# Optimization experiments

Measured on AMD Instinct MI355X. Metric: run time of the kernel, lower is better.

The kernel has to match this reference:

```python
import jax, jax.numpy as jnp
import numpy as np

B, T, D = 2, 2048, 2048
H = 16
D_HEAD = D // H          # 128
D_SUB = D_HEAD // 2      # 64
SCALE = float(np.sqrt(D_SUB))


def setup_inputs() -> dict:
    key = jax.random.key(0)
    ks = jax.random.split(key, 6)
    s = 1.0 / np.sqrt(D)
    return {
        "x": jax.random.normal(ks[0], (B, T, D), dtype=jnp.float32),
        "W_q": jax.random.normal(ks[1], (D, D), dtype=jnp.float32) * s,
        "W_k": jax.random.normal(ks[2], (D, D), dtype=jnp.float32) * s,
        "W_v": jax.random.normal(ks[3], (D, D), dtype=jnp.float32) * s,
        "W_o": jax.random.normal(ks[4], (D, D), dtype=jnp.float32) * s,
        "lambda_param": jnp.full((H,), 0.8, dtype=jnp.float32),
    }


def reference(x, W_q, W_k, W_v, W_o, lambda_param):
    # Linear layers (torch nn.Linear: x @ W.T), reshape to heads
    Q = (x @ W_q.T).reshape(B, T, H, D_HEAD)
    K = (x @ W_k.T).reshape(B, T, H, D_HEAD)
    V = (x @ W_v.T).reshape(B, T, H, D_HEAD)
    # split each head into two sub-heads
    Q1, Q2 = Q[..., :D_SUB], Q[..., D_SUB:2 * D_SUB]
    K1, K2 = K[..., :D_SUB], K[..., D_SUB:2 * D_SUB]
    # dual attention maps: [B, H, T, T]
    attn1 = jnp.einsum('bthd,bshd->bhts', Q1, K1) / SCALE
    attn2 = jnp.einsum('bthd,bshd->bhts', Q2, K2) / SCALE
    A1 = jax.nn.softmax(attn1, axis=-1)
    A2 = jax.nn.softmax(attn2, axis=-1)
    lam = jax.nn.sigmoid(lambda_param)[None, :, None, None]  # [1,H,1,1]
    A_diff = A1 - lam * A2
    # weighted values -> [B, T, H, d_head] -> [B, T, D]
    out = jnp.einsum('bhts,bshd->bthd', A_diff, V).reshape(B, T, D)
    return out @ W_o.T
```

## Files before the change

kernel.cpp:

```cpp
#include <hip/hip_runtime.h>
#include <math.h>

#define B_  2
#define T_  2048
#define D_  2048
#define H_  16
#define DH  128
#define BT  (B_ * T_)

typedef float    f32x4 __attribute__((ext_vector_type(4)));
typedef _Float16 f16x8 __attribute__((ext_vector_type(8)));
typedef __fp16   fp16x2 __attribute__((ext_vector_type(2)));

typedef __attribute__((address_space(1))) const void* gas_t;
typedef __attribute__((address_space(3))) void*       las_t;

__device__ __forceinline__ void gll16(const void* g, void* l) {
    __builtin_amdgcn_global_load_lds((gas_t)g, (las_t)l, 16, 0, 0);
}

__device__ __forceinline__ unsigned short h16bits(float f) {
    union { _Float16 h; unsigned short u; } c; c.h = (_Float16)f; return c.u;
}
__device__ __forceinline__ unsigned pk2h(float a, float b) {
    union { fp16x2 h; unsigned u; } c;
    c.h = __builtin_amdgcn_cvt_pkrtz(a, b);
    return c.u;
}

__global__ __launch_bounds__(256)
void f32_to_f16_multi(const float* __restrict__ s0, _Float16* __restrict__ d0, int n0,
                      const float* __restrict__ s1, _Float16* __restrict__ d1, int n1,
                      const float* __restrict__ s2, _Float16* __restrict__ d2, int n2,
                      const float* __restrict__ s3, _Float16* __restrict__ d3, int n3) {
    const float* s; _Float16* d; int n;
    switch (blockIdx.y) {
        case 0:  s = s0; d = d0; n = n0; break;
        case 1:  s = s1; d = d1; n = n1; break;
        case 2:  s = s2; d = d2; n = n2; break;
        default: s = s3; d = d3; n = n3; break;
    }
    int i = blockIdx.x * 256 + threadIdx.x;
    if (i >= n) return;
    const float4 a = *(const float4*)(s + (size_t)i * 8);
    const float4 b = *(const float4*)(s + (size_t)i * 8 + 4);
    f16x8 o;
    o[0] = (_Float16)a.x; o[1] = (_Float16)a.y; o[2] = (_Float16)a.z; o[3] = (_Float16)a.w;
    o[4] = (_Float16)b.x; o[5] = (_Float16)b.y; o[6] = (_Float16)b.z; o[7] = (_Float16)b.w;
    *(f16x8*)(d + (size_t)i * 8) = o;
}

__global__ __launch_bounds__(256)
void f32_to_f16(const float* __restrict__ in, _Float16* __restrict__ out, int n8) {
    int i = blockIdx.x * 256 + threadIdx.x;
    if (i >= n8) return;
    const float4 a = *(const float4*)(in + (size_t)i * 8);
    const float4 b = *(const float4*)(in + (size_t)i * 8 + 4);
    f16x8 o;
    o[0] = (_Float16)a.x; o[1] = (_Float16)a.y; o[2] = (_Float16)a.z; o[3] = (_Float16)a.w;
    o[4] = (_Float16)b.x; o[5] = (_Float16)b.y; o[6] = (_Float16)b.z; o[7] = (_Float16)b.w;
    *(f16x8*)(out + (size_t)i * 8) = o;
}

#define BKK 64

template<int EPI>
__global__ __launch_bounds__(256, 3)
void gemm16(const _Float16* __restrict__ Ag, const _Float16* __restrict__ Bg,
            float* __restrict__ Cf, _Float16* __restrict__ C16,
            _Float16* __restrict__ Vt, int M, int N, int K, float oscale) {
    __shared__ _Float16 As[128 * BKK];
    __shared__ _Float16 Bs[128 * BKK];

    const int tid  = threadIdx.x;
    const int lane = tid & 63;
    const int w    = tid >> 6;
    const int wr   = w >> 1, wc = w & 1;
    const int c    = lane & 15, g = lane >> 4;

    const int nwg = gridDim.x;
    const int bid = blockIdx.x;
    const int swz = (bid & 7) * (nwg >> 3) + (bid >> 3);
    const int nb  = N / 128;
    const int bm  = (swz / nb) * 128;
    const int bn  = (swz % nb) * 128;

    const int srow = tid >> 3;
    const int sg   = (tid & 7) ^ (srow & 7);
    const _Float16* Ab = Ag + (size_t)(bm + srow) * K + sg * 8;
    const _Float16* Bb = Bg + (size_t)(bn + srow) * K + sg * 8;

    f32x4 acc[4][4];
    #pragma unroll
    for (int mi = 0; mi < 4; ++mi)
        #pragma unroll
        for (int ni = 0; ni < 4; ++ni)
            #pragma unroll
            for (int r = 0; r < 4; ++r) acc[mi][ni][r] = 0.f;

    for (int k0 = 0; k0 < K; k0 += BKK) {
        __syncthreads();
        #pragma unroll
        for (int i = 0; i < 4; ++i) {
            gll16(Ab + (size_t)i * 32 * K + k0, &As[(i * 256 + tid) * 8]);
            gll16(Bb + (size_t)i * 32 * K + k0, &Bs[(i * 256 + tid) * 8]);
        }
        __syncthreads();

        #pragma unroll
        for (int kc = 0; kc < 2; ++kc) {
            f16x8 fa[4], fb[4];
            #pragma unroll
            for (int mi = 0; mi < 4; ++mi) {
                const int row = wr * 64 + mi * 16 + c;
                fa[mi] = *(const f16x8*)&As[row * 64 + (((kc * 4 + g) ^ (c & 7)) * 8)];
            }
            #pragma unroll
            for (int ni = 0; ni < 4; ++ni) {
                const int row = wc * 64 + ni * 16 + c;
                fb[ni] = *(const f16x8*)&Bs[row * 64 + (((kc * 4 + g) ^ (c & 7)) * 8)];
            }
            #pragma unroll
            for (int mi = 0; mi < 4; ++mi)
                #pragma unroll
                for (int ni = 0; ni < 4; ++ni)
                    acc[mi][ni] = __builtin_amdgcn_mfma_f32_16x16x32_f16(fa[mi], fb[ni], acc[mi][ni], 0, 0, 0);
        }
    }

    #pragma unroll
    for (int mi = 0; mi < 4; ++mi) {
        #pragma unroll
        for (int ni = 0; ni < 4; ++ni) {
            const int m0 = bm + wr * 64 + mi * 16 + g * 4;
            const int n  = bn + wc * 64 + ni * 16 + c;
            if constexpr (EPI == 0) {
                #pragma unroll
                for (int r = 0; r < 4; ++r)
                    Cf[(size_t)(m0 + r) * N + n] = acc[mi][ni][r];
            } else if constexpr (EPI == 1) {
                #pragma unroll
                for (int r = 0; r < 4; ++r)
                    C16[(size_t)(m0 + r) * N + n] = (_Float16)(acc[mi][ni][r] * oscale);
            } else {
                const int bb = m0 >> 11, t = m0 & (T_ - 1);
                ushort4 o;
                o.x = h16bits(acc[mi][ni][0]); o.y = h16bits(acc[mi][ni][1]);
                o.z = h16bits(acc[mi][ni][2]); o.w = h16bits(acc[mi][ni][3]);
                *(ushort4*)&Vt[((size_t)bb * D_ + n) * T_ + t] = o;
            }
        }
    }
}

#define QB  64
#define KVB 64

__device__ __forceinline__ void softmax_upd(f32x4 s[4], float& l,
                                            unsigned pk[4][2]) {
    float e[4][4];
    #pragma unroll
    for (int mt = 0; mt < 4; ++mt) {
        #pragma unroll
        for (int r = 0; r < 4; ++r) e[mt][r] = exp2f(s[mt][r]);
        pk[mt][0] = pk2h(e[mt][0], e[mt][1]);
        pk[mt][1] = pk2h(e[mt][2], e[mt][3]);
    }
    float tsum = 0.f;
    #pragma unroll
    for (int mt = 0; mt < 4; ++mt)
        #pragma unroll
        for (int r = 0; r < 4; ++r) tsum += e[mt][r];
    tsum += __shfl_xor(tsum, 16);
    tsum += __shfl_xor(tsum, 32);
    l += tsum;
}

__global__ __launch_bounds__(256, 2)
void diff_attn_f16(_Float16* Qh,
                   const _Float16* __restrict__ Kh,
                   const _Float16* __restrict__ Vt,
                   const float* __restrict__ lambda_param) {
    __shared__ __align__(16) char smem[64 * 1024];
    float* ob = (float*)smem;

    const int tid  = threadIdx.x;
    const int lane = tid & 63;
    const int w    = tid >> 6;
    const int qsub = w >> 1;
    const int path = w & 1;
    const int b    = blockIdx.z, h = blockIdx.y;
    const int t0   = blockIdx.x * QB;
    const int c    = lane & 15;
    const int g    = lane >> 4;

    const float lam = 1.f / (1.f + __expf(-lambda_param[h]));

    const int q0 = t0 + qsub * 32;
    const _Float16* Qg = Qh + (size_t)(b * T_ + q0 + c) * D_ + h * DH + path * 64;
    f16x8 qf[2][2];
    #pragma unroll
    for (int qh = 0; qh < 2; ++qh) {
        qf[qh][0] = *(const f16x8*)&Qg[(size_t)qh * 16 * D_ + g * 8];
        qf[qh][1] = *(const f16x8*)&Qg[(size_t)qh * 16 * D_ + 32 + g * 8];
    }

    f32x4 O[2][8];
    #pragma unroll
    for (int qh = 0; qh < 2; ++qh)
        #pragma unroll
        for (int nt = 0; nt < 8; ++nt)
            #pragma unroll
            for (int r = 0; r < 4; ++r) O[qh][nt][r] = 0.f;
    float l[2] = {0.f, 0.f};

    const int kkey = tid >> 4;
    const int kgs  = (tid & 15) ^ (kkey & 7);
    const int vd   = tid >> 3;
    const int vgs  = (tid & 7) ^ (vd & 7);
    const char* kp[4];
    const char* vp[4];
    #pragma unroll
    for (int i = 0; i < 4; ++i) {
        kp[i] = (const char*)(Kh + ((size_t)(b * T_ + i * 16 + kkey)) * D_ + h * DH + kgs * 8);
        vp[i] = (const char*)(Vt + ((size_t)(b * D_ + h * DH + i * 32 + vd)) * T_ + vgs * 8);
    }
    const size_t KADV = (size_t)KVB * D_ * sizeof(_Float16);
    const size_t VADV = (size_t)KVB * sizeof(_Float16);

    auto STAGE = [&](int buf) {
        char* kb_ = smem + (size_t)buf * 16384;
        char* vb_ = smem + 32768 + (size_t)buf * 16384;
        #pragma unroll
        for (int i = 0; i < 4; ++i) {
            gll16(kp[i], kb_ + (size_t)(i * 256 + tid) * 16);
            gll16(vp[i], vb_ + (size_t)(i * 256 + tid) * 16);
            kp[i] += KADV; vp[i] += VADV;
        }
    };

    STAGE(0);

    const int NT = T_ / KVB;
    for (int t = 0; t < NT; ++t) {
        const int cur = t & 1;
        __syncthreads();
        if (t + 1 < NT) STAGE(cur ^ 1);

        const _Float16* k_s = (const _Float16*)(smem + (size_t)cur * 16384);
        const _Float16* v_s = (const _Float16*)(smem + 32768 + (size_t)cur * 16384);

        f32x4 s[2][4];
        #pragma unroll
        for (int qh = 0; qh < 2; ++qh)
            #pragma unroll
            for (int mt = 0; mt < 4; ++mt)
                #pragma unroll
                for (int r = 0; r < 4; ++r) s[qh][mt][r] = 0.f;
        __builtin_amdgcn_s_setprio(1);
        #pragma unroll
        for (int mt = 0; mt < 4; ++mt) {
            const int key  = mt * 16 + c;
            const int krow = key * 128;
            #pragma unroll
            for (int kb = 0; kb < 2; ++kb) {
                const int gp = ((path * 8 + kb * 4 + g) ^ (key & 7)) * 8;
                f16x8 kf = *(const f16x8*)&k_s[krow + gp];
                s[0][mt] = __builtin_amdgcn_mfma_f32_16x16x32_f16(kf, qf[0][kb], s[0][mt], 0, 0, 0);
                s[1][mt] = __builtin_amdgcn_mfma_f32_16x16x32_f16(kf, qf[1][kb], s[1][mt], 0, 0, 0);
            }
        }
        __builtin_amdgcn_s_setprio(0);

        unsigned pk[2][4][2];
        softmax_upd(s[0], l[0], pk[0]);
        softmax_upd(s[1], l[1], pk[1]);

        const int srcA = ((2 * (g & 1)) << 4) | c;
        const int srcB = ((2 * (g & 1) + 1) << 4) | c;
        const bool hiSel = (g & 2) != 0;
        #pragma unroll
        for (int kb = 0; kb < 2; ++kb) {
            f16x8 vf[8];
            #pragma unroll
            for (int nt = 0; nt < 8; ++nt) {
                const int d  = nt * 16 + c;
                const int gp = ((4 * kb + g) ^ (d & 7)) * 8;
                vf[nt] = *(const f16x8*)&v_s[d * 64 + gp];
            }
            #pragma unroll
            for (int qh = 0; qh < 2; ++qh) {
                unsigned u00 = (unsigned)__shfl((int)pk[qh][2 * kb][0], srcA);
                unsigned u10 = (unsigned)__shfl((int)pk[qh][2 * kb + 1][0], srcA);
                unsigned u01 = (unsigned)__shfl((int)pk[qh][2 * kb][1], srcA);
                unsigned u11 = (unsigned)__shfl((int)pk[qh][2 * kb + 1][1], srcA);
                unsigned u02 = (unsigned)__shfl((int)pk[qh][2 * kb][0], srcB);
                unsigned u12 = (unsigned)__shfl((int)pk[qh][2 * kb + 1][0], srcB);
                unsigned u03 = (unsigned)__shfl((int)pk[qh][2 * kb][1], srcB);
                unsigned u13 = (unsigned)__shfl((int)pk[qh][2 * kb + 1][1], srcB);
                union { unsigned u[4]; f16x8 v; } pa;
                pa.u[0] = hiSel ? u10 : u00;
                pa.u[1] = hiSel ? u11 : u01;
                pa.u[2] = hiSel ? u12 : u02;
                pa.u[3] = hiSel ? u13 : u03;
                __builtin_amdgcn_s_setprio(1);
                #pragma unroll
                for (int nt = 0; nt < 8; ++nt)
                    O[qh][nt] = __builtin_amdgcn_mfma_f32_16x16x32_f16(pa.v, vf[nt], O[qh][nt], 0, 0, 0);
                __builtin_amdgcn_s_setprio(0);
            }
        }
    }

    float il[2][4];
    #pragma unroll
    for (int qh = 0; qh < 2; ++qh)
        #pragma unroll
        for (int r = 0; r < 4; ++r) {
            float L = __shfl(l[qh], (g << 2) | r);
            il[qh][r] = (path ? lam : 1.f) / L;
        }

    __syncthreads();
    if (path) {
        float* obp = ob + (size_t)(qsub * 32) * 132;
        #pragma unroll
        for (int qh = 0; qh < 2; ++qh)
            #pragma unroll
            for (int nt = 0; nt < 8; ++nt)
                #pragma unroll
                for (int r = 0; r < 4; ++r)
                    obp[(qh * 16 + g * 4 + r) * 132 + nt * 16 + c] = O[qh][nt][r] * il[qh][r];
    }
    __syncthreads();
    if (!path) {
        const float* obp = ob + (size_t)(qsub * 32) * 132;
        const size_t obase = (size_t)(b * T_ + q0) * D_ + h * DH;
        #pragma unroll
        for (int qh = 0; qh < 2; ++qh)
            #pragma unroll
            for (int nt = 0; nt < 8; ++nt)
                #pragma unroll
                for (int r = 0; r < 4; ++r) {
                    float o = O[qh][nt][r] * il[qh][r]
                            - obp[(qh * 16 + g * 4 + r) * 132 + nt * 16 + c];
                    Qh[obase + (size_t)(qh * 16 + g * 4 + r) * D_ + nt * 16 + c] = (_Float16)o;
                }
    }
}

extern "C" void kernel_launch(void* const* d_in, const int* in_sizes, int n_in,
                              void* d_out, int out_size, void* d_ws, size_t ws_size,
                              hipStream_t stream) {
    const float* x    = (const float*)d_in[0];
    const float* W_q  = (const float*)d_in[1];
    const float* W_k  = (const float*)d_in[2];
    const float* W_v  = (const float*)d_in[3];
    const float* W_o  = (const float*)d_in[4];
    const float* lamp = (const float*)d_in[5];
    float* out = (float*)d_out;

    const size_t PL = (size_t)BT * D_;
    const size_t WL = (size_t)D_ * D_;
    _Float16* Xh = (_Float16*)d_ws;
    _Float16* Wq = Xh + PL;
    _Float16* Wk = Wq + WL;
    _Float16* Wv = Wk + WL;
    _Float16* Qh = Wv + WL;
    _Float16* Kh = Qh + PL;
    _Float16* Vt = Kh + PL;
    _Float16* Wo = Wq;

    const float C1 = 0.125f * 1.44269504089f;

    dim3 gc((unsigned)(PL / 8 + 255) / 256, 4);
    f32_to_f16_multi<<<gc, 256, 0, stream>>>(x,   Xh, (int)(PL / 8),
                                             W_q, Wq, (int)(WL / 8),
                                             W_k, Wk, (int)(WL / 8),
                                             W_v, Wv, (int)(WL / 8));

    dim3 gg(512);
    gemm16<1><<<gg, 256, 0, stream>>>(Xh, Wq, nullptr, Qh, nullptr, BT, D_, D_, C1);
    gemm16<1><<<gg, 256, 0, stream>>>(Xh, Wk, nullptr, Kh, nullptr, BT, D_, D_, 1.f);
    gemm16<2><<<gg, 256, 0, stream>>>(Xh, Wv, nullptr, nullptr, Vt, BT, D_, D_, 1.f);

    f32_to_f16<<<(int)(WL / 8 / 256), 256, 0, stream>>>(W_o, Wo, (int)(WL / 8));

    dim3 ga(T_ / QB, H_, B_);
    diff_attn_f16<<<ga, 256, 0, stream>>>(Qh, Kh, Vt, lamp);

    gemm16<0><<<gg, 256, 0, stream>>>(Qh, Wo, out, nullptr, nullptr, BT, D_, D_, 1.f);
}
```

Baseline: 347.6 us.

## Merge QKV GEMMs into one launch, fold W_o conversion, shrink attention LDS

Runs the three QKV projection GEMMs as one launch with a grid y-dimension, and converts W_o inside the multi-tensor conversion kernel, which removes several launches and tail effects. The attention kernel drops its LDS double buffer in favor of register prefetch into a single 32KB buffer, and stores the output exchange in fp16. This lets occupancy rise from 2 to 3 blocks per CU. Row-sum shuffles are deferred from every KV tile to the epilogue. In exchange, global-to-LDS copy overlap is lost, register pressure rises, and the exchanged lambda-scaled output loses some precision.

```diff
diff --git a/kernel.cpp b/kernel.cpp
--- a/kernel.cpp
+++ b/kernel.cpp
@@ -32,13 +32,15 @@
 void f32_to_f16_multi(const float* __restrict__ s0, _Float16* __restrict__ d0, int n0,
                       const float* __restrict__ s1, _Float16* __restrict__ d1, int n1,
                       const float* __restrict__ s2, _Float16* __restrict__ d2, int n2,
-                      const float* __restrict__ s3, _Float16* __restrict__ d3, int n3) {
+                      const float* __restrict__ s3, _Float16* __restrict__ d3, int n3,
+                      const float* __restrict__ s4, _Float16* __restrict__ d4, int n4) {
     const float* s; _Float16* d; int n;
     switch (blockIdx.y) {
         case 0:  s = s0; d = d0; n = n0; break;
         case 1:  s = s1; d = d1; n = n1; break;
         case 2:  s = s2; d = d2; n = n2; break;
-        default: s = s3; d = d3; n = n3; break;
+        case 3:  s = s3; d = d3; n = n3; break;
+        default: s = s4; d = d4; n = n4; break;
     }
     int i = blockIdx.x * 256 + threadIdx.x;
     if (i >= n) return;
@@ -50,27 +52,57 @@
     *(f16x8*)(d + (size_t)i * 8) = o;
 }
 
-__global__ __launch_bounds__(256)
-void f32_to_f16(const float* __restrict__ in, _Float16* __restrict__ out, int n8) {
-    int i = blockIdx.x * 256 + threadIdx.x;
-    if (i >= n8) return;
-    const float4 a = *(const float4*)(in + (size_t)i * 8);
-    const float4 b = *(const float4*)(in + (size_t)i * 8 + 4);
-    f16x8 o;
-    o[0] = (_Float16)a.x; o[1] = (_Float16)a.y; o[2] = (_Float16)a.z; o[3] = (_Float16)a.w;
-    o[4] = (_Float16)b.x; o[5] = (_Float16)b.y; o[6] = (_Float16)b.z; o[7] = (_Float16)b.w;
-    *(f16x8*)(out + (size_t)i * 8) = o;
-}
-
 #define BKK 64
 
-template<int EPI>
+__device__ __forceinline__ void gemm_body(const _Float16* Ab, const _Float16* Bb,
+                                          _Float16* As, _Float16* Bs,
+                                          f32x4 acc[4][4], int K, int tid,
+                                          int c, int g, int wr, int wc) {
+    for (int k0 = 0; k0 < K; k0 += BKK) {
+        __syncthreads();
+        #pragma unroll
+        for (int i = 0; i < 4; ++i) {
+            gll16(Ab + (size_t)i * 32 * K + k0, &As[(i * 256 + tid) * 8]);
+            gll16(Bb + (size_t)i * 32 * K + k0, &Bs[(i * 256 + tid) * 8]);
+        }
+        __syncthreads();
+        #pragma unroll
+        for (int kc = 0; kc < 2; ++kc) {
+            f16x8 fa[4], fb[4];
+            #pragma unroll
+            for (int mi = 0; mi < 4; ++mi) {
+                const int row = wr * 64 + mi * 16 + c;
+                fa[mi] = *(const f16x8*)&As[row * 64 + (((kc * 4 + g) ^ (c & 7)) * 8)];
+            }
+            #pragma unroll
+            for (int ni = 0; ni < 4; ++ni) {
+                const int row = wc * 64 + ni * 16 + c;
+                fb[ni] = *(const f16x8*)&Bs[row * 64 + (((kc * 4 + g) ^ (c & 7)) * 8)];
+            }
+            #pragma unroll
+            for (int mi = 0; mi < 4; ++mi)
+                #pragma unroll
+                for (int ni = 0; ni < 4; ++ni)
+                    acc[mi][ni] = __builtin_amdgcn_mfma_f32_16x16x32_f16(fa[mi], fb[ni], acc[mi][ni], 0, 0, 0);
+        }
+    }
+}
+
 __global__ __launch_bounds__(256, 3)
-void gemm16(const _Float16* __restrict__ Ag, const _Float16* __restrict__ Bg,
-            float* __restrict__ Cf, _Float16* __restrict__ C16,
-            _Float16* __restrict__ Vt, int M, int N, int K, float oscale) {
+void gemm16_qkv(const _Float16* __restrict__ Xh,
+                const _Float16* __restrict__ Wq, const _Float16* __restrict__ Wk,
+                const _Float16* __restrict__ Wv,
+                _Float16* __restrict__ Qh, _Float16* __restrict__ Kh,
+                _Float16* __restrict__ Vt, int M, int N, int K, float c1) {
     __shared__ _Float16 As[128 * BKK];
     __shared__ _Float16 Bs[128 * BKK];
+
+    const _Float16* Bg; _Float16* C16; float osc = 1.f; int epi;
+    switch (blockIdx.y) {
+        case 0:  Bg = Wq; C16 = Qh; osc = c1; epi = 1; break;
+        case 1:  Bg = Wk; C16 = Kh; epi = 1; break;
+        default: Bg = Wv; C16 = Vt; epi = 2; break;
+    }
 
     const int tid  = threadIdx.x;
     const int lane = tid & 63;
@@ -87,7 +119,7 @@
 
     const int srow = tid >> 3;
     const int sg   = (tid & 7) ^ (srow & 7);
-    const _Float16* Ab = Ag + (size_t)(bm + srow) * K + sg * 8;
+    const _Float16* Ab = Xh + (size_t)(bm + srow) * K + sg * 8;
     const _Float16* Bb = Bg + (size_t)(bn + srow) * K + sg * 8;
 
     f32x4 acc[4][4];
@@ -98,35 +130,7 @@
             #pragma unroll
             for (int r = 0; r < 4; ++r) acc[mi][ni][r] = 0.f;
 
-    for (int k0 = 0; k0 < K; k0 += BKK) {
-        __syncthreads();
-        #pragma unroll
-        for (int i = 0; i < 4; ++i) {
-            gll16(Ab + (size_t)i * 32 * K + k0, &As[(i * 256 + tid) * 8]);
-            gll16(Bb + (size_t)i * 32 * K + k0, &Bs[(i * 256 + tid) * 8]);
-        }
-        __syncthreads();
-
-        #pragma unroll
-        for (int kc = 0; kc < 2; ++kc) {
-            f16x8 fa[4], fb[4];
-            #pragma unroll
-            for (int mi = 0; mi < 4; ++mi) {
-                const int row = wr * 64 + mi * 16 + c;
-                fa[mi] = *(const f16x8*)&As[row * 64 + (((kc * 4 + g) ^ (c & 7)) * 8)];
-            }
-            #pragma unroll
-            for (int ni = 0; ni < 4; ++ni) {
-                const int row = wc * 64 + ni * 16 + c;
-                fb[ni] = *(const f16x8*)&Bs[row * 64 + (((kc * 4 + g) ^ (c & 7)) * 8)];
-            }
-            #pragma unroll
-            for (int mi = 0; mi < 4; ++mi)
-                #pragma unroll
-                for (int ni = 0; ni < 4; ++ni)
-                    acc[mi][ni] = __builtin_amdgcn_mfma_f32_16x16x32_f16(fa[mi], fb[ni], acc[mi][ni], 0, 0, 0);
-        }
-    }
+    gemm_body(Ab, Bb, As, Bs, acc, K, tid, c, g, wr, wc);
 
     #pragma unroll
     for (int mi = 0; mi < 4; ++mi) {
@@ -134,23 +138,65 @@
         for (int ni = 0; ni < 4; ++ni) {
             const int m0 = bm + wr * 64 + mi * 16 + g * 4;
             const int n  = bn + wc * 64 + ni * 16 + c;
-            if constexpr (EPI == 0) {
+            if (epi == 1) {
                 #pragma unroll
                 for (int r = 0; r < 4; ++r)
-                    Cf[(size_t)(m0 + r) * N + n] = acc[mi][ni][r];
-            } else if constexpr (EPI == 1) {
-                #pragma unroll
-                for (int r = 0; r < 4; ++r)
-                    C16[(size_t)(m0 + r) * N + n] = (_Float16)(acc[mi][ni][r] * oscale);
+                    C16[(size_t)(m0 + r) * N + n] = (_Float16)(acc[mi][ni][r] * osc);
             } else {
                 const int bb = m0 >> 11, t = m0 & (T_ - 1);
                 ushort4 o;
                 o.x = h16bits(acc[mi][ni][0]); o.y = h16bits(acc[mi][ni][1]);
                 o.z = h16bits(acc[mi][ni][2]); o.w = h16bits(acc[mi][ni][3]);
-                *(ushort4*)&Vt[((size_t)bb * D_ + n) * T_ + t] = o;
-            }
-        }
-    }
+                *(ushort4*)&C16[((size_t)bb * D_ + n) * T_ + t] = o;
+            }
+        }
+    }
+}
+
+__global__ __launch_bounds__(256, 3)
+void gemm16_f32(const _Float16* __restrict__ Ag, const _Float16* __restrict__ Bg,
+                float* __restrict__ Cf, int M, int N, int K) {
+    __shared__ _Float16 As[128 * BKK];
+    __shared__ _Float16 Bs[128 * BKK];
+
+    const int tid  = threadIdx.x;
+    const int lane = tid & 63;
+    const int w    = tid >> 6;
+    const int wr   = w >> 1, wc = w & 1;
+    const int c    = lane & 15, g = lane >> 4;
+
+    const int nwg = gridDim.x;
+    const int bid = blockIdx.x;
+    const int swz = (bid & 7) * (nwg >> 3) + (bid >> 3);
+    const int nb  = N / 128;
+    const int bm  = (swz / nb) * 128;
+    const int bn  = (swz % nb) * 128;
+
+    const int srow = tid >> 3;
+    const int sg   = (tid & 7) ^ (srow & 7);
+    const _Float16* Ab = Ag + (size_t)(bm + srow) * K + sg * 8;
+    const _Float16* Bb = Bg + (size_t)(bn + srow) * K + sg * 8;
+
+    f32x4 acc[4][4];
+    #pragma unroll
+    for (int mi = 0; mi < 4; ++mi)
+        #pragma unroll
+        for (int ni = 0; ni < 4; ++ni)
+            #pragma unroll
+            for (int r = 0; r < 4; ++r) acc[mi][ni][r] = 0.f;
+
+    gemm_body(Ab, Bb, As, Bs, acc, K, tid, c, g, wr, wc);
+
+    #pragma unroll
+    for (int mi = 0; mi < 4; ++mi)
+        #pragma unroll
+        for (int ni = 0; ni < 4; ++ni) {
+            const int m0 = bm + wr * 64 + mi * 16 + g * 4;
+            const int n  = bn + wc * 64 + ni * 16 + c;
+            #pragma unroll
+            for (int r = 0; r < 4; ++r)
+                Cf[(size_t)(m0 + r) * N + n] = acc[mi][ni][r];
+        }
 }
 
 #define QB  64
@@ -171,18 +217,18 @@
     for (int mt = 0; mt < 4; ++mt)
         #pragma unroll
         for (int r = 0; r < 4; ++r) tsum += e[mt][r];
-    tsum += __shfl_xor(tsum, 16);
-    tsum += __shfl_xor(tsum, 32);
     l += tsum;
 }
 
-__global__ __launch_bounds__(256, 2)
+__global__ __launch_bounds__(256, 3)
 void diff_attn_f16(_Float16* Qh,
                    const _Float16* __restrict__ Kh,
                    const _Float16* __restrict__ Vt,
                    const float* __restrict__ lambda_param) {
-    __shared__ __align__(16) char smem[64 * 1024];
-    float* ob = (float*)smem;
+    __shared__ __align__(16) char smem[32 * 1024];
+    _Float16* k_s = (_Float16*)smem;
+    _Float16* v_s = (_Float16*)(smem + 16384);
+    _Float16* ob  = (_Float16*)smem;
 
     const int tid  = threadIdx.x;
     const int lane = tid & 63;
@@ -228,27 +274,31 @@
     const size_t KADV = (size_t)KVB * D_ * sizeof(_Float16);
     const size_t VADV = (size_t)KVB * sizeof(_Float16);
 
-    auto STAGE = [&](int buf) {
-        char* kb_ = smem + (size_t)buf * 16384;
-        char* vb_ = smem + 32768 + (size_t)buf * 16384;
-        #pragma unroll
-        for (int i = 0; i < 4; ++i) {
-            gll16(kp[i], kb_ + (size_t)(i * 256 + tid) * 16);
-            gll16(vp[i], vb_ + (size_t)(i * 256 + tid) * 16);
-            kp[i] += KADV; vp[i] += VADV;
-        }
-    };
-
-    STAGE(0);
+    uint4 kreg[4], vreg[4];
+    #pragma unroll
+    for (int i = 0; i < 4; ++i) {
+        kreg[i] = *(const uint4*)kp[i];
+        vreg[i] = *(const uint4*)vp[i];
+        kp[i] += KADV; vp[i] += VADV;
+    }
 
     const int NT = T_ / KVB;
     for (int t = 0; t < NT; ++t) {
-        const int cur = t & 1;
         __syncthreads();
-        if (t + 1 < NT) STAGE(cur ^ 1);
-
-        const _Float16* k_s = (const _Float16*)(smem + (size_t)cur * 16384);
-        const _Float16* v_s = (const _Float16*)(smem + 32768 + (size_t)cur * 16384);
+        #pragma unroll
+        for (int i = 0; i < 4; ++i) {
+            *(uint4*)&k_s[(size_t)(i * 256 + tid) * 8] = kreg[i];
+            *(uint4*)&v_s[(size_t)(i * 256 + tid) * 8] = vreg[i];
+        }
+        if (t + 1 < NT) {
+            #pragma unroll
+            for (int i = 0; i < 4; ++i) {
+                kreg[i] = *(const uint4*)kp[i];
+                vreg[i] = *(const uint4*)vp[i];
+                kp[i] += KADV; vp[i] += VADV;
+            }
+        }
+        __syncthreads();
 
         f32x4 s[2][4];
         #pragma unroll
@@ -317,24 +367,27 @@
     for (int qh = 0; qh < 2; ++qh)
         #pragma unroll
         for (int r = 0; r < 4; ++r) {
-            float L = __shfl(l[qh], (g << 2) | r);
+            const int src = (g << 2) | r;
+            float L = __shfl(l[qh], src)      + __shfl(l[qh], src + 16)
+                    + __shfl(l[qh], src + 32) + __shfl(l[qh], src + 48);
             il[qh][r] = (path ? lam : 1.f) / L;
         }
 
     __syncthreads();
     if (path) {
-        float* obp = ob + (size_t)(qsub * 32) * 132;
+        _Float16* obp = ob + (size_t)(qsub * 32) * 132;
         #pragma unroll
         for (int qh = 0; qh < 2; ++qh)
             #pragma unroll
             for (int nt = 0; nt < 8; ++nt)
                 #pragma unroll
                 for (int r = 0; r < 4; ++r)
-                    obp[(qh * 16 + g * 4 + r) * 132 + nt * 16 + c] = O[qh][nt][r] * il[qh][r];
+                    obp[(qh * 16 + g * 4 + r) * 132 + nt * 16 + c] =
+                        (_Float16)(O[qh][nt][r] * il[qh][r]);
     }
     __syncthreads();
     if (!path) {
-        const float* obp = ob + (size_t)(qsub * 32) * 132;
+        const _Float16* obp = ob + (size_t)(qsub * 32) * 132;
         const size_t obase = (size_t)(b * T_ + q0) * D_ + h * DH;
         #pragma unroll
         for (int qh = 0; qh < 2; ++qh)
@@ -343,7 +396,7 @@
                 #pragma unroll
                 for (int r = 0; r < 4; ++r) {
                     float o = O[qh][nt][r] * il[qh][r]
-                            - obp[(qh * 16 + g * 4 + r) * 132 + nt * 16 + c];
+                            - (float)obp[(qh * 16 + g * 4 + r) * 132 + nt * 16 + c];
                     Qh[obase + (size_t)(qh * 16 + g * 4 + r) * D_ + nt * 16 + c] = (_Float16)o;
                 }
     }
@@ -366,28 +419,25 @@
     _Float16* Wq = Xh + PL;
     _Float16* Wk = Wq + WL;
     _Float16* Wv = Wk + WL;
-    _Float16* Qh = Wv + WL;
+    _Float16* Wo = Wv + WL;
+    _Float16* Qh = Wo + WL;
     _Float16* Kh = Qh + PL;
     _Float16* Vt = Kh + PL;
-    _Float16* Wo = Wq;
 
     const float C1 = 0.125f * 1.44269504089f;
 
-    dim3 gc((unsigned)(PL / 8 + 255) / 256, 4);
+    dim3 gc((unsigned)(PL / 8 + 255) / 256, 5);
     f32_to_f16_multi<<<gc, 256, 0, stream>>>(x,   Xh, (int)(PL / 8),
                                              W_q, Wq, (int)(WL / 8),
                                              W_k, Wk, (int)(WL / 8),
-                                             W_v, Wv, (int)(WL / 8));
-
-    dim3 gg(512);
-    gemm16<1><<<gg, 256, 0, stream>>>(Xh, Wq, nullptr, Qh, nullptr, BT, D_, D_, C1);
-    gemm16<1><<<gg, 256, 0, stream>>>(Xh, Wk, nullptr, Kh, nullptr, BT, D_, D_, 1.f);
-    gemm16<2><<<gg, 256, 0, stream>>>(Xh, Wv, nullptr, nullptr, Vt, BT, D_, D_, 1.f);
-
-    f32_to_f16<<<(int)(WL / 8 / 256), 256, 0, stream>>>(W_o, Wo, (int)(WL / 8));
+                                             W_v, Wv, (int)(WL / 8),
+                                             W_o, Wo, (int)(WL / 8));
+
+    dim3 gq(512, 3);
+    gemm16_qkv<<<gq, 256, 0, stream>>>(Xh, Wq, Wk, Wv, Qh, Kh, Vt, BT, D_, D_, C1);
 
     dim3 ga(T_ / QB, H_, B_);
     diff_attn_f16<<<ga, 256, 0, stream>>>(Qh, Kh, Vt, lamp);
 
-    gemm16<0><<<gg, 256, 0, stream>>>(Qh, Wo, out, nullptr, nullptr, BT, D_, D_, 1.f);
-}
+    gemm16_f32<<<dim3(512), 256, 0, stream>>>(Qh, Wo, out, BT, D_, D_);
+}
```

After: 667.5 us. 92.1% more time.
